# Performance work log

Hardware: AMD Instinct MI355X
Metric: run time of the kernel (lower is better)

Reference implementation:

```python
import jax, jax.numpy as jnp
import numpy as np

ALPHA = 0.2
BETA = 1.0
TEMPERATURE = 0.05
EPS = 1e-8  # torch cosine_similarity eps


def setup_inputs() -> dict:
    key = jax.random.key(0)
    k1, k2 = jax.random.split(key)
    B, R, D = 4096, 18, 256  # rows, segment size (1 anchor + 1 pos + 16 negs), embed dim
    features = jax.random.normal(k1, (B * R, D), dtype=jnp.float32)
    scores = jax.random.normal(k2, (B * (R - 1),), dtype=jnp.float32)
    row_sizes = jnp.full((B,), R, dtype=jnp.int32)  # uniform ragged sizes
    logit_scale = jnp.array([1.0 / TEMPERATURE], dtype=jnp.float32)
    return {"features": features, "scores": scores, "row_sizes": row_sizes,
            "logit_scale": logit_scale}


def reference(features, scores, row_sizes, logit_scale):
    B = row_sizes.shape[0]
    R = features.shape[0] // B  # uniform segment size
    D = features.shape[1]
    f3 = features.reshape(B, R, D)
    anchor = f3[:, 0]          # [B, D]
    tgt = f3[:, 1:]            # [B, R-1, D]  (positive first, then negatives)

    # --- per-row cosine sims + log_softmax + KLDiv(batchmean) ---
    an = jnp.maximum(jnp.linalg.norm(anchor, axis=-1, keepdims=True), EPS)  # [B,1]
    tn = jnp.maximum(jnp.linalg.norm(tgt, axis=-1), EPS)                    # [B,R-1]
    cos = jnp.einsum('bd,bkd->bk', anchor, tgt) / (an * tn)                 # [B,R-1]
    emb_log = jax.nn.log_softmax(cos, axis=-1)                              # [B,R-1]
    ce = jax.nn.softmax(scores.reshape(B, R - 1), axis=-1)                  # [B,R-1]
    # torch KLDivLoss(reduction='batchmean') on a length-(R-1) vector divides by (R-1)
    kl = jnp.sum(ce * (jnp.log(ce) - emb_log), axis=-1) / (R - 1)           # [B]
    loss = jnp.mean(BETA * kl)

    # --- single InfoNCE over all rows: anchors vs [positives; all negatives] ---
    pos = f3[:, 1]                                   # [B, D]
    negs = f3[:, 2:].reshape(B * (R - 2), D)         # [B*(R-2), D]
    targets = jnp.concatenate([pos, negs], axis=0)   # [B*(R-1), D]
    logits = logit_scale[0] * (anchor @ targets.T)   # [B, B*(R-1)]
    labels = jnp.arange(B)
    # cross_entropy(logits, labels) with mean reduction
    infonce = jnp.mean(jax.nn.logsumexp(logits, axis=-1) - logits[labels, labels])

    return loss + ALPHA * infonce
```

## Files before the change

### kernel.cpp

```cpp
#include <hip/hip_runtime.h>
#include <math.h>

#define ALPHA 0.2f
#define BETA 1.0f
#define EPSV 1e-8f
#define LOG2E 1.4426950408889634f
#define LN2 0.6931471805599453f

#define BATCH 4096
#define RR 18
#define KT 17
#define DD 256
#define NTGT (BATCH*KT)
#define NTILE (NTGT/32)
#define TILE_BYTES (32*DD)

#define AG 64
#define NSPLIT 32
#define TPS (NTILE/NSPLIT)

#define EXPA 8388608.0f
#define EXPB 1064880320.0f

typedef int   i32x8  __attribute__((ext_vector_type(8)));
typedef float f32x16 __attribute__((ext_vector_type(16)));

__device__ inline int pk8(float a, float b, float c, float d){
  int p = __builtin_amdgcn_cvt_pk_fp8_f32(a, b, 0, false);
  return  __builtin_amdgcn_cvt_pk_fp8_f32(c, d, p, true);
}

__device__ inline float fmax3(float a, float b, float c){
  return fmaxf(fmaxf(a, b), c);
}

__device__ inline float fexp2u(float x, float kc){
  float t = fmaf(x, EXPA, kc);
  unsigned u;
  asm("v_cvt_u32_f32 %0, %1" : "=v"(u) : "v"(t));
  return __uint_as_float(u);
}


__global__ __launch_bounds__(256) void prep_kernel(
    const float* __restrict__ feat, const float* __restrict__ scores,
    const float* __restrict__ lscale,
    unsigned char* __restrict__ abf8, unsigned char* __restrict__ tbf8,
    float* __restrict__ diag, float* __restrict__ klarr,
    float* __restrict__ out){
  __shared__ float csh[KT];
  int b = blockIdx.x, tid = threadIdx.x;
  int grp = tid >> 4, j = tid & 15;
  const float* fb = feat + (size_t)b * RR * DD;
  float s2 = lscale[0] * LOG2E;

  if (b == 0 && tid == 0) out[0] = 0.f;

  float4 a0 = ((const float4*)fb)[j*4+0];
  float4 a1 = ((const float4*)fb)[j*4+1];
  float4 a2 = ((const float4*)fb)[j*4+2];
  float4 a3 = ((const float4*)fb)[j*4+3];
  float asq = (a0.x*a0.x+a0.y*a0.y+a0.z*a0.z+a0.w*a0.w)
            + (a1.x*a1.x+a1.y*a1.y+a1.z*a1.z+a1.w*a1.w)
            + (a2.x*a2.x+a2.y*a2.y+a2.z*a2.z+a2.w*a2.w)
            + (a3.x*a3.x+a3.y*a3.y+a3.z*a3.z+a3.w*a3.w);
  #pragma unroll
  for (int off=1; off<16; off<<=1) asq += __shfl_xor(asq, off);
  float an = fmaxf(sqrtf(asq), EPSV);

  if (tid < 16){
    uint4 v = make_uint4(
      (unsigned)pk8(a0.x*s2,a0.y*s2,a0.z*s2,a0.w*s2),
      (unsigned)pk8(a1.x*s2,a1.y*s2,a1.z*s2,a1.w*s2),
      (unsigned)pk8(a2.x*s2,a2.y*s2,a2.z*s2,a2.w*s2),
      (unsigned)pk8(a3.x*s2,a3.y*s2,a3.z*s2,a3.w*s2));
    *(uint4*)(abf8 + (size_t)b*DD + j*16) = v;
  }

  for (int kr = grp+1; kr <= KT; kr += 16){
    const float4* tp = (const float4*)(fb + (size_t)kr*DD) + j*4;
    float4 t0=tp[0], t1=tp[1], t2=tp[2], t3=tp[3];
    int t  = b*KT + (kr-1);
    int tile = t >> 5, m = t & 31;
    int ki = j >> 2, hf = (j >> 1) & 1, w = j & 1;
    uint4 v = make_uint4(
      (unsigned)pk8(t0.x,t0.y,t0.z,t0.w), (unsigned)pk8(t1.x,t1.y,t1.z,t1.w),
      (unsigned)pk8(t2.x,t2.y,t2.z,t2.w), (unsigned)pk8(t3.x,t3.y,t3.z,t3.w));
    *(uint4*)(tbf8 + (size_t)tile*TILE_BYTES + ki*2048 + w*1024 + hf*512 + m*16) = v;
    float d = (a0.x*t0.x+a0.y*t0.y+a0.z*t0.z+a0.w*t0.w)
            + (a1.x*t1.x+a1.y*t1.y+a1.z*t1.z+a1.w*t1.w)
            + (a2.x*t2.x+a2.y*t2.y+a2.z*t2.z+a2.w*t2.w)
            + (a3.x*t3.x+a3.y*t3.y+a3.z*t3.z+a3.w*t3.w);
    float q = (t0.x*t0.x+t0.y*t0.y+t0.z*t0.z+t0.w*t0.w)
            + (t1.x*t1.x+t1.y*t1.y+t1.z*t1.z+t1.w*t1.w)
            + (t2.x*t2.x+t2.y*t2.y+t2.z*t2.z+t2.w*t2.w)
            + (t3.x*t3.x+t3.y*t3.y+t3.z*t3.z+t3.w*t3.w);
    #pragma unroll
    for (int off=1; off<16; off<<=1){ d += __shfl_xor(d,off); q += __shfl_xor(q,off); }
    if (j == 0){
      csh[kr-1] = d / (an * fmaxf(sqrtf(q), EPSV));
      if (kr == 1) diag[b] = d;
    }
  }
  __syncthreads();

  if (tid < 64){
    bool act = tid < KT;
    float c  = act ? csh[tid] : -INFINITY;
    float sv = act ? scores[(size_t)b*KT + tid] : -INFINITY;
    float cm = c, sm = sv;
    #pragma unroll
    for (int off=1; off<64; off<<=1){
      cm = fmaxf(cm, __shfl_xor(cm, off));
      sm = fmaxf(sm, __shfl_xor(sm, off));
    }
    float ec = act ? __builtin_amdgcn_exp2f((c -cm)*LOG2E) : 0.f;
    float es = act ? __builtin_amdgcn_exp2f((sv-sm)*LOG2E) : 0.f;
    float cs = ec, ss = es;
    #pragma unroll
    for (int off=1; off<64; off<<=1){
      cs += __shfl_xor(cs, off);
      ss += __shfl_xor(ss, off);
    }
    float lse_c = cm + __logf(cs);
    float lse_s = sm + __logf(ss);
    float kt = 0.f;
    if (act){
      float lq = sv - lse_s;
      float lp = c  - lse_c;
      kt = __builtin_amdgcn_exp2f(lq*LOG2E)*(lq - lp);
    }
    #pragma unroll
    for (int off=1; off<64; off<<=1) kt += __shfl_xor(kt, off);
    if (tid == 0) klarr[b] = kt * (1.0f/KT);
  }
}

__global__ __launch_bounds__(64,2) void gemm_lse_kernel(
    const unsigned char* __restrict__ abf8, const unsigned char* __restrict__ tbf8,
    float* __restrict__ part_m, float* __restrict__ part_s){
  const int bid  = blockIdx.x;
  const int ns   = (bid & 7)*4 + ((bid >> 3) & 3);
  const int ag   = bid >> 5;
  const int lane = threadIdx.x;
  const int l31  = lane & 31;
  const int half = lane >> 5;

  i32x8 af[2][4];
  {
    const unsigned char* ab = abf8 + (size_t)ag*64*DD;
    #pragma unroll
    for (int nt=0;nt<2;++nt)
      #pragma unroll
      for (int ki=0;ki<4;++ki){
        const unsigned char* p = ab + (size_t)(nt*32+l31)*DD + ki*64 + half*32;
        uint4 lo = *(const uint4*)p;
        uint4 hi = *(const uint4*)(p+16);
        af[nt][ki] = (i32x8){(int)lo.x,(int)lo.y,(int)lo.z,(int)lo.w,
                             (int)hi.x,(int)hi.y,(int)hi.z,(int)hi.w};
      }
  }

  const unsigned char* gbase =
      tbf8 + (size_t)(ns*TPS)*TILE_BYTES + half*512 + l31*16;

  i32x8 ta[4], tb[4];
  auto ld = [&](int tt, i32x8 tf[4]){
    const unsigned char* p = gbase + (size_t)tt*TILE_BYTES;
    #pragma unroll
    for (int ki=0;ki<4;++ki){
      uint4 lo = *(const uint4*)(p + ki*2048);
      uint4 hi = *(const uint4*)(p + ki*2048 + 1024);
      tf[ki] = (i32x8){(int)lo.x,(int)lo.y,(int)lo.z,(int)lo.w,
                       (int)hi.x,(int)hi.y,(int)hi.z,(int)hi.w};
    }
  };

  float run_m[2] = {-INFINITY,-INFINITY};
  float run_s[2] = {0.f,0.f};
  f32x16 acc[2];

  auto mfma_tile = [&](i32x8 tf[4]){
    acc[0] = (f32x16)(0.f);
    acc[1] = (f32x16)(0.f);
    __builtin_amdgcn_s_setprio(1);
    #pragma unroll
    for (int ki=0;ki<4;++ki){
      acc[0] = __builtin_amdgcn_mfma_scale_f32_32x32x64_f8f6f4(
                   tf[ki], af[0][ki], acc[0], 0,0, 0,127, 0,127);
      acc[1] = __builtin_amdgcn_mfma_scale_f32_32x32x64_f8f6f4(
                   tf[ki], af[1][ki], acc[1], 0,0, 0,127, 0,127);
    }
    __builtin_amdgcn_s_setprio(0);
  };

  auto epilogue = [&](){
    #pragma unroll
    for (int nt=0;nt<2;++nt){
      f32x16 t = acc[nt];
      float x0 = fmax3(t[0], t[1], t[2]);
      float x1 = fmax3(t[3], t[4], t[5]);
      float x2 = fmax3(t[6], t[7], t[8]);
      float x3 = fmax3(t[9], t[10], t[11]);
      float x4 = fmax3(t[12], t[13], t[14]);
      float mx = fmaxf(fmax3(x0,x1,x2), fmax3(x3,x4,t[15]));

      float kc = fmaf(mx, -EXPA, EXPB);
      float s0=0.f, s1=0.f, s2=0.f, s3=0.f;
      #pragma unroll
      for (int r=0;r<16;r+=4){
        s0 += fexp2u(t[r  ],kc);
        s1 += fexp2u(t[r+1],kc);
        s2 += fexp2u(t[r+2],kc);
        s3 += fexp2u(t[r+3],kc);
      }
      float sh = (s0+s1)+(s2+s3);

      float nm = fmaxf(run_m[nt], mx);
      run_s[nt] = run_s[nt]*__builtin_amdgcn_exp2f(run_m[nt]-nm)
                + sh*__builtin_amdgcn_exp2f(mx-nm);
      run_m[nt] = nm;
    }
  };

  ld(0, ta);
  ld(1, tb);
  for (int t=0; t<TPS; t+=2){
    mfma_tile(ta);
    if (t+2 < TPS) ld(t+2, ta);
    epilogue();
    mfma_tile(tb);
    if (t+3 < TPS) ld(t+3, tb);
    epilogue();
  }

  #pragma unroll
  for (int nt=0;nt<2;++nt){
    float om = __shfl_xor(run_m[nt], 32);
    float os = __shfl_xor(run_s[nt], 32);
    float nm = fmaxf(run_m[nt], om);
    float S  = run_s[nt]*__builtin_amdgcn_exp2f(run_m[nt]-nm)
             + os*__builtin_amdgcn_exp2f(om-nm);
    if (half == 0){
      int gm = ag*64 + nt*32 + l31;
      part_m[(size_t)ns*BATCH + gm] = nm;
      part_s[(size_t)ns*BATCH + gm] = S;
    }
  }
}

__global__ __launch_bounds__(256) void combine_kernel(
    const float* __restrict__ part_m, const float* __restrict__ part_s,
    const float* __restrict__ diag, const float* __restrict__ klarr,
    const float* __restrict__ lscale, float* __restrict__ out){
  int tid = threadIdx.x;
  int b = blockIdx.x*256 + tid;
  float s = lscale[0];
  float m = -INFINITY, S = 0.f;
  #pragma unroll
  for (int ns=0; ns<NSPLIT; ++ns){
    float pm_ = part_m[(size_t)ns*BATCH + b];
    float ps_ = part_s[(size_t)ns*BATCH + b];
    float nm = fmaxf(m, pm_);
    S = S*__builtin_amdgcn_exp2f(m-nm) + ps_*__builtin_amdgcn_exp2f(pm_-nm);
    m = nm;
  }
  float inf = (m + __log2f(S))*LN2 - s*diag[b];
  float c = BETA*klarr[b] + ALPHA*inf;
  #pragma unroll
  for (int off=1; off<64; off<<=1) c += __shfl_xor(c, off);
  if ((tid & 63) == 0) atomicAdd(out, c*(1.0f/BATCH));
}

extern "C" void kernel_launch(void* const* d_in, const int* in_sizes, int n_in,
                              void* d_out, int out_size, void* d_ws, size_t ws_size,
                              hipStream_t stream){
  const float* feat   = (const float*)d_in[0];
  const float* scores = (const float*)d_in[1];
  const float* lscale = (const float*)d_in[3];

  float* ws     = (float*)d_ws;
  float* diag   = ws;
  float* klarr  = diag + BATCH;
  float* part_m = klarr + BATCH;
  float* part_s = part_m + (size_t)NSPLIT*BATCH;
  unsigned char* abf8 = (unsigned char*)(part_s + (size_t)NSPLIT*BATCH);
  unsigned char* tbf8 = abf8 + (size_t)BATCH*DD;

  float* outp = (float*)d_out;
  prep_kernel<<<BATCH, 256, 0, stream>>>(feat, scores, lscale, abf8, tbf8,
                                         diag, klarr, outp);
  gemm_lse_kernel<<<AG*NSPLIT, 64, 0, stream>>>(abf8, tbf8, part_m, part_s);
  combine_kernel<<<BATCH/256, 256, 0, stream>>>(part_m, part_s, diag, klarr,
                                                lscale, outp);
}
```

Measured before the change: 190.0 us.

## Share target tiles across four waves via LDS ring with async global-to-LDS loads

The GEMM+logsumexp kernel now runs 256-thread blocks in which four waves each own 64 anchor rows. The target fp8 tiles are staged once per block into a 4-slot LDS ring using global_load_lds, replacing per-wave direct global loads. This cuts global/L2 traffic for the target matrix by a factor of four. The accumulators are double-buffered so MFMA on one tile overlaps the exp epilogue of the previous one. The cost is block-wide barriers on every tile and fewer blocks in flight (512 instead of 2048).

Result: no change. 188.0 us (-1.1%).

```diff
diff --git a/kernel.cpp b/kernel.cpp
--- a/kernel.cpp
+++ b/kernel.cpp
@@ -15,15 +15,22 @@
 #define NTILE (NTGT/32)
 #define TILE_BYTES (32*DD)
 
-#define AG 64
+#define AG 16
 #define NSPLIT 32
 #define TPS (NTILE/NSPLIT)
+#define NRING 4
 
 #define EXPA 8388608.0f
 #define EXPB 1064880320.0f
 
 typedef int   i32x8  __attribute__((ext_vector_type(8)));
 typedef float f32x16 __attribute__((ext_vector_type(16)));
+
+__device__ inline void gl_lds16(const void* g, void* l){
+  __builtin_amdgcn_global_load_lds(
+      (const __attribute__((address_space(1))) unsigned int*)g,
+      (__attribute__((address_space(3))) unsigned int*)l, 16, 0, 0);
+}
 
 __device__ inline int pk8(float a, float b, float c, float d){
   int p = __builtin_amdgcn_cvt_pk_fp8_f32(a, b, 0, false);
@@ -136,19 +143,36 @@
   }
 }
 
-__global__ __launch_bounds__(64,2) void gemm_lse_kernel(
+__global__ __launch_bounds__(256,2) void gemm_lse_kernel(
     const unsigned char* __restrict__ abf8, const unsigned char* __restrict__ tbf8,
     float* __restrict__ part_m, float* __restrict__ part_s){
+  __shared__ __align__(16) unsigned char Bs[NRING][TILE_BYTES];
   const int bid  = blockIdx.x;
   const int ns   = (bid & 7)*4 + ((bid >> 3) & 3);
   const int ag   = bid >> 5;
-  const int lane = threadIdx.x;
+  const int tid  = threadIdx.x;
+  const int lane = tid & 63;
+  const int wave = tid >> 6;
   const int l31  = lane & 31;
   const int half = lane >> 5;
 
+  const unsigned char* gbase = tbf8 + (size_t)(ns*TPS)*TILE_BYTES;
+  auto stage = [&](int t){
+    const unsigned char* g = gbase + (size_t)t*TILE_BYTES;
+    unsigned char* l = &Bs[t & (NRING-1)][0];
+    #pragma unroll
+    for (int jj=0;jj<2;++jj){
+      int off = jj*4096 + tid*16;
+      gl_lds16(g + off, l + off);
+    }
+  };
+
+  stage(0);
+  stage(1);
+
   i32x8 af[2][4];
   {
-    const unsigned char* ab = abf8 + (size_t)ag*64*DD;
+    const unsigned char* ab = abf8 + (size_t)(ag*256 + wave*64)*DD;
     #pragma unroll
     for (int nt=0;nt<2;++nt)
       #pragma unroll
@@ -161,28 +185,28 @@
       }
   }
 
-  const unsigned char* gbase =
-      tbf8 + (size_t)(ns*TPS)*TILE_BYTES + half*512 + l31*16;
-
-  i32x8 ta[4], tb[4];
-  auto ld = [&](int tt, i32x8 tf[4]){
-    const unsigned char* p = gbase + (size_t)tt*TILE_BYTES;
+  float run_m[2] = {-INFINITY,-INFINITY};
+  float run_s[2] = {0.f,0.f};
+  f32x16 accA[2], accB[2];
+  #pragma unroll
+  for (int nt=0;nt<2;++nt){ accA[nt]=(f32x16)(0.f); accB[nt]=(f32x16)(0.f); }
+
+  auto mfma_tile = [&](int t, f32x16 (&acc)[2], bool last){
+    if (last) asm volatile("s_waitcnt vmcnt(0)" ::: "memory");
+    else      asm volatile("s_waitcnt vmcnt(2)" ::: "memory");
+    __builtin_amdgcn_s_barrier();
+    asm volatile("" ::: "memory");
+    if (t+2 < TPS) stage(t+2);
+
+    const unsigned char* fb = &Bs[t & (NRING-1)][0] + half*512 + l31*16;
+    i32x8 tf[4];
     #pragma unroll
     for (int ki=0;ki<4;++ki){
-      uint4 lo = *(const uint4*)(p + ki*2048);
-      uint4 hi = *(const uint4*)(p + ki*2048 + 1024);
+      uint4 lo = *(const uint4*)(fb + ki*2048);
+      uint4 hi = *(const uint4*)(fb + ki*2048 + 1024);
       tf[ki] = (i32x8){(int)lo.x,(int)lo.y,(int)lo.z,(int)lo.w,
                        (int)hi.x,(int)hi.y,(int)hi.z,(int)hi.w};
     }
-  };
-
-  float run_m[2] = {-INFINITY,-INFINITY};
-  float run_s[2] = {0.f,0.f};
-  f32x16 acc[2];
-
-  auto mfma_tile = [&](i32x8 tf[4]){
-    acc[0] = (f32x16)(0.f);
-    acc[1] = (f32x16)(0.f);
     __builtin_amdgcn_s_setprio(1);
     #pragma unroll
     for (int ki=0;ki<4;++ki){
@@ -194,7 +218,7 @@
     __builtin_amdgcn_s_setprio(0);
   };
 
-  auto epilogue = [&](){
+  auto epilogue = [&](f32x16 (&acc)[2]){
     #pragma unroll
     for (int nt=0;nt<2;++nt){
       f32x16 t = acc[nt];
@@ -220,19 +244,20 @@
       run_s[nt] = run_s[nt]*__builtin_amdgcn_exp2f(run_m[nt]-nm)
                 + sh*__builtin_amdgcn_exp2f(mx-nm);
       run_m[nt] = nm;
+      acc[nt] = (f32x16)(0.f);
     }
   };
 
-  ld(0, ta);
-  ld(1, tb);
-  for (int t=0; t<TPS; t+=2){
-    mfma_tile(ta);
-    if (t+2 < TPS) ld(t+2, ta);
-    epilogue();
-    mfma_tile(tb);
-    if (t+3 < TPS) ld(t+3, tb);
-    epilogue();
-  }
+  mfma_tile(0, accA, false);
+  for (int t=1; t+1 < TPS; t+=2){
+    mfma_tile(t,   accB, false);
+    epilogue(accA);
+    mfma_tile(t+1, accA, false);
+    epilogue(accB);
+  }
+  mfma_tile(TPS-1, accB, true);
+  epilogue(accA);
+  epilogue(accB);
 
   #pragma unroll
   for (int nt=0;nt<2;++nt){
@@ -242,7 +267,7 @@
     float S  = run_s[nt]*__builtin_amdgcn_exp2f(run_m[nt]-nm)
              + os*__builtin_amdgcn_exp2f(om-nm);
     if (half == 0){
-      int gm = ag*64 + nt*32 + l31;
+      int gm = ag*256 + wave*64 + nt*32 + l31;
       part_m[(size_t)ns*BATCH + gm] = nm;
       part_s[(size_t)ns*BATCH + gm] = S;
     }
@@ -290,7 +315,7 @@
   float* outp = (float*)d_out;
   prep_kernel<<<BATCH, 256, 0, stream>>>(feat, scores, lscale, abf8, tbf8,
                                          diag, klarr, outp);
-  gemm_lse_kernel<<<AG*NSPLIT, 64, 0, stream>>>(abf8, tbf8, part_m, part_s);
+  gemm_lse_kernel<<<AG*NSPLIT, 256, 0, stream>>>(abf8, tbf8, part_m, part_s);
   combine_kernel<<<BATCH/256, 256, 0, stream>>>(part_m, part_s, diag, klarr,
                                                 lscale, outp);
 }
```
